# Performance work log

Measured on AMD Instinct MI355X. Metric: run time of the kernel, lower is better.

Reference implementation:

```python
import jax, jax.numpy as jnp
import numpy as np

B, S, T, H, E, V = 64, 128, 64, 512, 256, 10000


def setup_inputs() -> dict:
    key = jax.random.key(0)
    ks = jax.random.split(key, 16)
    w = 0.05
    return {
        "trg": jax.random.randint(ks[0], (B, T), 0, V),
        "encoder_hidden": jax.random.normal(ks[1], (B, S, 2 * H), jnp.float32),
        "src_lengths": jax.random.randint(ks[2], (B,), 1, S + 1),
        "h0": jax.random.normal(ks[3], (B, H), jnp.float32),
        "c0": jax.random.normal(ks[4], (B, H), jnp.float32),
        "emb_table": jax.random.normal(ks[5], (V, E), jnp.float32) * w,
        "Wkey": jax.random.normal(ks[6], (2 * H, H), jnp.float32) * w,      # attention.key_layer
        "Wquery": jax.random.normal(ks[7], (H, H), jnp.float32) * w,        # attention.query_layer
        "we": jax.random.normal(ks[8], (H,), jnp.float32) * w,              # attention.energy_layer
        "W_ih": jax.random.normal(ks[9], (4 * H, E + 2 * H), jnp.float32) * w,
        "W_hh": jax.random.normal(ks[10], (4 * H, H), jnp.float32) * w,
        "b_ih": jnp.zeros((4 * H,), jnp.float32),
        "b_hh": jnp.zeros((4 * H,), jnp.float32),
        "Wpre": jax.random.normal(ks[11], (3 * H + E, H), jnp.float32) * w,  # pre_output_layer (no bias)
        "Wgen": jax.random.normal(ks[12], (H, V), jnp.float32) * w,          # generator / softmax head
    }


def reference(trg, encoder_hidden, src_lengths, h0, c0, emb_table, Wkey, Wquery,
              we, W_ih, W_hh, b_ih, b_hh, Wpre, Wgen):
    # Teacher-forced unroll (teacher_forcing=True branch); dropout in eval mode.
    s = encoder_hidden.shape[1]
    proj_key = encoder_hidden @ Wkey                            # [B,S,H]
    mask = jnp.arange(s)[None, :] < src_lengths[:, None]        # [B,S]
    embs = emb_table[trg]                                       # [B,T,E]

    def step(carry, emb_t):
        h, c = carry                                            # [B,H] each
        q = h @ Wquery                                          # query = last-layer hidden
        e = jnp.einsum('bsh,h->bs', jnp.tanh(q[:, None, :] + proj_key), we)
        a = jax.nn.softmax(jnp.where(mask, e, -1e9), axis=-1)   # masked attention
        ctx = jnp.einsum('bs,bsd->bd', a, encoder_hidden)       # [B,2H]
        x = jnp.concatenate([emb_t, ctx], axis=-1)              # rnn_input
        g = x @ W_ih.T + h @ W_hh.T + b_ih + b_hh
        i_g, f_g, g_g, o_g = jnp.split(g, 4, axis=-1)           # torch LSTM gate order
        c_new = jax.nn.sigmoid(f_g) * c + jax.nn.sigmoid(i_g) * jnp.tanh(g_g)
        h_new = jax.nn.sigmoid(o_g) * jnp.tanh(c_new)
        pre = jnp.concatenate([emb_t, h_new, ctx], axis=-1) @ Wpre
        logp = jax.nn.log_softmax(pre @ Wgen, axis=-1)          # [B,V]
        return (h_new, c_new), logp

    (hf, cf), out = jax.lax.scan(step, (h0, c0), jnp.swapaxes(embs, 0, 1))
    return jnp.transpose(out, (1, 2, 0)), hf, cf                # out: [B,V,T]
```

## Files before the change

### kernel.cpp

```cpp
#include <hip/hip_runtime.h>

#define B 64
#define S 128
#define T 64
#define H 512
#define E 256
#define V 10000
#define H2 1024
#define G4 2048
#define KX 1536
#define KP 1792
#define VP 10112
#define NROW 4096

typedef unsigned short u16;
typedef __attribute__((ext_vector_type(8))) short bf16x8;
typedef __attribute__((ext_vector_type(4))) short bf16x4;
typedef __attribute__((ext_vector_type(4))) float floatx4;

__device__ inline float b2f(u16 h){
  union { unsigned int u; float f; } v; v.u = ((unsigned int)h) << 16; return v.f;
}
__device__ inline u16 f2b(float f){
  union { unsigned int u; float f; } v; v.f = f;
  unsigned int r = v.u + 0x7FFFu + ((v.u >> 16) & 1u);
  return (u16)(r >> 16);
}
__device__ __forceinline__ float rcpf(float x){ return __builtin_amdgcn_rcpf(x); }
__device__ inline float sigf(float x){ return rcpf(1.f + __expf(-x)); }
__device__ inline float tanh_fast(float x){ float e=__expf(2.f*x); return 1.f - 2.f*rcpf(e+1.f); }

__device__ __forceinline__ void st_wt_u32(u16* p, unsigned v){
  asm volatile("global_store_dword %0, %1, off sc0 sc1" :: "v"(p), "v"(v) : "memory");
}
__device__ __forceinline__ void st_wt_u16(u16* p, unsigned v){
  asm volatile("global_store_short %0, %1, off sc0 sc1" :: "v"(p), "v"(v) : "memory");
}
__device__ __forceinline__ unsigned ld_if(unsigned* p){
  unsigned v;
  asm volatile("global_load_dword %0, %1, off sc0 sc1\ns_waitcnt vmcnt(0)" : "=v"(v) : "v"(p) : "memory");
  return v;
}
__device__ __forceinline__ void st_if(unsigned* p, unsigned v){
  asm volatile("global_store_dword %0, %1, off sc0 sc1\ns_waitcnt vmcnt(0)" :: "v"(p), "v"(v) : "memory");
}

#define BAR_WORDS (128*64)

__global__ void k_cast(const float* __restrict__ src, u16* __restrict__ dst, int n){
  int i = blockIdx.x*256 + threadIdx.x;
  if (i < n) dst[i] = f2b(src[i]);
}
__global__ void k_tct(const float* __restrict__ src, u16* __restrict__ dst, int R, int C){
  __shared__ float tile[64][65];
  int c0 = blockIdx.x*64, r0 = blockIdx.y*64;
  int tid = threadIdx.x;
  #pragma unroll
  for (int i=0;i<16;i++){
    int flat = i*256 + tid;
    int rr = flat >> 6, cc = flat & 63;
    int c = c0 + cc;
    tile[rr][cc] = (c < C) ? src[(size_t)(r0+rr)*C + c] : 0.f;
  }
  __syncthreads();
  #pragma unroll
  for (int i=0;i<16;i++){
    int flat = i*256 + tid;
    int cc = flat >> 6, rr = flat & 63;
    dst[(size_t)(c0+cc)*R + r0 + rr] = f2b(tile[rr][cc]);
  }
}
__global__ void k_wch(const float* __restrict__ wih, const float* __restrict__ whh, u16* __restrict__ o){
  int i = blockIdx.x*256 + threadIdx.x;
  if (i < G4*KX){
    int gp = i / KX, k = i % KX;
    int j = gp >> 2, gate = gp & 3, g = gate*H + j;
    float v = (k < H2) ? wih[(size_t)g*(E+H2) + E + k] : whh[(size_t)g*H + (k - H2)];
    o[i] = f2b(v);
  }
}
__global__ void k_wihe(const float* __restrict__ wih, u16* __restrict__ o){
  int i = blockIdx.x*256 + threadIdx.x;
  if (i < G4*E){
    int gp = i / E, e = i % E;
    int j = gp >> 2, gate = gp & 3, g = gate*H + j;
    o[i] = f2b(wih[(size_t)g*(E+H2) + e]);
  }
}
__global__ void k_bias(const float* __restrict__ bi, const float* __restrict__ bh, float* __restrict__ o){
  int i = blockIdx.x*256 + threadIdx.x;
  if (i < G4){
    int j = i >> 2, gate = i & 3, g = gate*H + j;
    o[i] = bi[g] + bh[g];
  }
}
__global__ void k_emb(const int* __restrict__ trg, const float* __restrict__ emb, u16* __restrict__ catp){
  int i = blockIdx.x*256 + threadIdx.x;
  if (i < NROW*E){
    int row = i >> 8, e = i & 255;
    int tok = trg[row];
    catp[(size_t)row*KP + e] = f2b(emb[(size_t)tok*E + e]);
  }
}
__global__ void k_init(const float* __restrict__ h0, u16* __restrict__ xgs){
  int i = blockIdx.x*256 + threadIdx.x;
  if (i < B*H){
    int b = i >> 9, j = i & 511;
    xgs[(size_t)b*KX + H2 + j] = f2b(h0[i]);
  }
}
__global__ void k_zero(unsigned* bar){
  int i = blockIdx.x*256 + threadIdx.x;
  if (i < BAR_WORDS) bar[i] = 0u;
}
__global__ void k_lse(const float* __restrict__ sep, float* __restrict__ lse){
  int r = blockIdx.x*256 + threadIdx.x;
  if (r < NROW){
    float s = 0.f;
    for (int i=0;i<79;i++) s += sep[(size_t)r*80 + i];
    lse[r] = logf(s);
  }
}

template<int TN, int EPI>
__global__ __launch_bounds__(256) void gemm_bf16(
    const u16* __restrict__ A, int lda,
    const u16* __restrict__ BT, int ldb,
    int K,
    u16* outb, int ldc,
    float* sep,
    float* outp, const float* lse)
{
  constexpr int NSUB = TN/16;
  constexpr int NB = TN/64;
  __shared__ u16 sA[64*32];
  __shared__ u16 sB[TN*32];
  __shared__ float Cx[(EPI==3) ? 128*65 : 1];
  __shared__ float lseb[(EPI==3)?64:1];

  const int tid = threadIdx.x;
  const int lane = tid & 63;
  const int wv = tid >> 6;
  const int row0 = blockIdx.x * 64;
  const int n0 = blockIdx.y * TN;

  floatx4 acc[NSUB];
  #pragma unroll
  for (int s=0;s<NSUB;s++) acc[s] = (floatx4){0.f,0.f,0.f,0.f};

  const int ar = tid >> 2;
  const int ch = tid & 3;
  const int swz = (ar >> 1) & 3;
  const int px = ((lane & 15) >> 1) & 3;

  const u16* gA = A + (size_t)(row0+ar)*lda + ch*8;
  bf16x8 pa = *(const bf16x8*)gA;
  bf16x8 pb[NB];
  #pragma unroll
  for (int i=0;i<NB;i++) pb[i] = *(const bf16x8*)(BT + (size_t)(n0+i*64+ar)*ldb + ch*8);

  for (int k0 = 0; k0 < K; k0 += 32){
    __syncthreads();
    *(bf16x8*)&sA[ar*32 + ((ch ^ swz)*8)] = pa;
    #pragma unroll
    for (int i=0;i<NB;i++)
      *(bf16x8*)&sB[(i*64+ar)*32 + ((ch ^ swz)*8)] = pb[i];
    __syncthreads();
    if (k0 + 32 < K){
      pa = *(const bf16x8*)(gA + k0 + 32);
      #pragma unroll
      for (int i=0;i<NB;i++) pb[i] = *(const bf16x8*)(BT + (size_t)(n0+i*64+ar)*ldb + k0+32 + ch*8);
    }
    bf16x8 af = *(const bf16x8*)&sA[(16*wv + (lane&15))*32 + (((lane>>4) ^ px)*8)];
    #pragma unroll
    for (int s=0;s<NSUB;s++){
      bf16x8 bfv = *(const bf16x8*)&sB[(16*s + (lane&15))*32 + (((lane>>4) ^ px)*8)];
      acc[s] = __builtin_amdgcn_mfma_f32_16x16x32_bf16(af, bfv, acc[s], 0, 0, 0);
    }
  }

  if constexpr (EPI == 0 || EPI == 4){
    #pragma unroll
    for (int s=0;s<NSUB;s++)
      #pragma unroll
      for (int r=0;r<4;r++){
        int row = row0 + 16*wv + ((lane>>4)<<2) + r;
        int col = n0 + 16*s + (lane&15);
        if (EPI == 4) row = ((row & 63) << 6) | (row >> 6);
        outb[(size_t)row*ldc + col] = f2b(acc[s][r]);
      }
  }
  if constexpr (EPI == 2){
    float sr[4] = {0.f,0.f,0.f,0.f};
    #pragma unroll
    for (int s=0;s<NSUB;s++){
      int col = n0 + 16*s + (lane&15);
      if (col < V){
        #pragma unroll
        for (int r=0;r<4;r++) sr[r] += __expf(acc[s][r]);
      }
    }
    #pragma unroll
    for (int r=0;r<4;r++){
      float v = sr[r];
      v += __shfl_xor(v,1); v += __shfl_xor(v,2); v += __shfl_xor(v,4); v += __shfl_xor(v,8);
      sr[r] = v;
    }
    if ((lane&15)==0){
      #pragma unroll
      for (int r=0;r<4;r++){
        int row = row0 + 16*wv + ((lane>>4)<<2) + r;
        sep[(size_t)row*80 + blockIdx.y] = sr[r];
      }
    }
  }
  if constexpr (EPI == 3){
    #pragma unroll
    for (int s=0;s<NSUB;s++)
      #pragma unroll
      for (int r=0;r<4;r++){
        int rl = 16*wv + ((lane>>4)<<2) + r;
        int cl = 16*s + (lane&15);
        Cx[cl*65 + rl] = acc[s][r];
      }
    if (tid < 64) lseb[tid] = lse[row0 + tid];
    __syncthreads();
    int b = blockIdx.x;
    for (int idx = tid; idx < TN*16; idx += 256){
      int vl = idx >> 4, q4 = idx & 15;
      int v = n0 + vl;
      if (v < V){
        floatx4 o;
        o[0] = Cx[vl*65 + q4*4+0] - lseb[q4*4+0];
        o[1] = Cx[vl*65 + q4*4+1] - lseb[q4*4+1];
        o[2] = Cx[vl*65 + q4*4+2] - lseb[q4*4+2];
        o[3] = Cx[vl*65 + q4*4+3] - lseb[q4*4+3];
        *(floatx4*)&outp[((size_t)b*V + v)*T + q4*4] = o;
      }
    }
  }
}

__device__ __forceinline__ void wait_flags(unsigned* base, unsigned g){
  if (threadIdx.x < 64){
    unsigned* p = base + (unsigned)threadIdx.x*64;
    int it = 0;
    while (ld_if(p) < g && ++it < 5000000) asm volatile("s_sleep 1":::);
  }
  __syncthreads();
}

__global__ __launch_bounds__(512) void decoder_loop(
    u16* __restrict__ xgs, const float* __restrict__ c0f, float* __restrict__ outp,
    const u16* __restrict__ pk, const u16* __restrict__ encb,
    const float* __restrict__ we, const int* __restrict__ lens,
    const u16* __restrict__ wqT, u16* __restrict__ cph,
    const u16* __restrict__ wch, const u16* __restrict__ gembt,
    const float* __restrict__ bias, unsigned* __restrict__ bar)
{
  __shared__ u16 sA[64*128];
  __shared__ u16 sB[32*128];
  __shared__ float Cx[64*36];
  __shared__ u16 hsb[H];
  __shared__ __align__(16) float qw[H];
  __shared__ __align__(16) float wel[H];
  __shared__ float ep[512];
  __shared__ float ev[S], al[S];
  __shared__ float smax, sinv;

  const int tid = threadIdx.x, lane = tid & 63, wv = tid >> 6;
  const int blk = blockIdx.x;
  const int xcd = blk & 7, slot = blk >> 3;
  unsigned* flag_ctx = bar;
  unsigned* flag_h   = bar + 64*64;

  if (slot < 8){
    const int b = xcd*8 + slot;
    const int lenb = lens[b];
    wel[tid] = we[tid];
    __syncthreads();

    for (int t=0; t<T; t++){
      wait_flags(flag_h, (unsigned)t);
      u16* xgt = xgs + (size_t)t*B*KX;
      hsb[tid] = xgt[b*KX + H2 + tid];
      __syncthreads();
      {
        floatx4 accq[4];
        #pragma unroll
        for (int s=0;s<4;s++) accq[s] = (floatx4){0.f,0.f,0.f,0.f};
        const int kc = (lane>>4)*8;
        #pragma unroll 4
        for (int ks=0; ks<16; ks++){
          bf16x8 af = *(const bf16x8*)&hsb[ks*32 + kc];
          #pragma unroll
          for (int s=0;s<4;s++){
            const u16* bp = wqT + (size_t)(wv*64 + s*16 + (lane&15))*H + ks*32 + kc;
            accq[s] = __builtin_amdgcn_mfma_f32_16x16x32_bf16(af, *(const bf16x8*)bp, accq[s], 0, 0, 0);
          }
        }
        if (lane < 16){
          #pragma unroll
          for (int s=0;s<4;s++) qw[wv*64 + s*16 + lane] = accq[s][0];
        }
      }
      __syncthreads();
      {
        int s = tid >> 2, part = tid & 3;
        float a0 = 0.f;
        if (s < lenb){
          const u16* pr = pk + (size_t)(b*S + s)*H;
          #pragma unroll 4
          for (int m=0;m<16;m++){
            int k0 = part*8 + m*32;
            bf16x8 p8 = *(const bf16x8*)(pr + k0);
            floatx4 qa = *(const floatx4*)&qw[k0];
            floatx4 qb = *(const floatx4*)&qw[k0+4];
            floatx4 wa = *(const floatx4*)&wel[k0];
            floatx4 wb = *(const floatx4*)&wel[k0+4];
            #pragma unroll
            for (int i=0;i<4;i++){
              a0 += tanh_fast(qa[i] + b2f((u16)p8[i]))   * wa[i];
              a0 += tanh_fast(qb[i] + b2f((u16)p8[i+4])) * wb[i];
            }
          }
        }
        ep[tid] = a0;
      }
      __syncthreads();
      if (tid < S){
        float e = ep[tid*4] + ep[tid*4+1] + ep[tid*4+2] + ep[tid*4+3];
        ev[tid] = (tid < lenb) ? e : -1e30f;
      }
      __syncthreads();
      if (tid < 64){
        float m = fmaxf(ev[tid], ev[tid+64]);
        #pragma unroll
        for (int o=32;o>=1;o>>=1) m = fmaxf(m, __shfl_xor(m,o));
        if (tid==0) smax = m;
      }
      __syncthreads();
      if (tid < S) al[tid] = __expf(ev[tid]-smax);
      __syncthreads();
      if (tid < 64){
        float s2 = al[tid] + al[tid+64];
        #pragma unroll
        for (int o=32;o>=1;o>>=1) s2 += __shfl_xor(s2,o);
        if (tid==0) sinv = rcpf(s2);
      }
      __syncthreads();
      {
        float cx0=0.f, cx1=0.f;
        int d = tid*2;
        const u16* er = encb + (size_t)(b*S)*H2 + d;
        for (int ss=0; ss<lenb; ss++){
          unsigned int u = *(const unsigned int*)(er + (size_t)ss*H2);
          float a = al[ss];
          cx0 += a * b2f((u16)(u & 0xFFFFu));
          cx1 += a * b2f((u16)(u >> 16));
        }
        cx0 *= sinv; cx1 *= sinv;
        unsigned pack = ((unsigned)f2b(cx1) << 16) | (unsigned)f2b(cx0);
        st_wt_u32(xgt + (size_t)b*KX + d, pack);
        *(unsigned*)&cph[(size_t)(b*T + t)*KP + E + H + d] = pack;
      }
      asm volatile("s_waitcnt vmcnt(0)" ::: "memory");
      __syncthreads();
      if (tid == 0) st_if(flag_ctx + (unsigned)b*64, (unsigned)(t+1));
      __syncthreads();
    }
  } else {
    const int g = slot - 8;
    const int gid = xcd*8 + g;
    const int n0 = xcd*256 + g*32;
    const int kh = wv >> 2, wr = wv & 3;
    const int rs0 = tid >> 4, gs = tid & 15;
    const int rowa = 16*wr + (lane & 15);
    const int pb_ = tid >> 3, jl = tid & 7;
    const int jglob = (n0 >> 2) + jl;
    float creg = c0f[pb_*H + jglob];
    floatx4 bias4 = *(const floatx4*)(bias + n0 + jl*4);

    for (int t=0; t<T; t++){
      wait_flags(flag_ctx, (unsigned)(t+1));
      const u16* xgt = xgs + (size_t)t*B*KX;
      u16* xgn = xgs + (size_t)(t+1)*B*KX;
      bf16x4 g4 = *(const bf16x4*)(gembt + (size_t)(t*B + pb_)*G4 + n0 + jl*4);

      floatx4 acc[2];
      acc[0] = (floatx4){0.f,0.f,0.f,0.f};
      acc[1] = (floatx4){0.f,0.f,0.f,0.f};
      bf16x8 a0 = *(const bf16x8*)(xgt + (size_t)rs0*KX + gs*8);
      bf16x8 a1 = *(const bf16x8*)(xgt + (size_t)(rs0+32)*KX + gs*8);
      bf16x8 b0 = *(const bf16x8*)(wch + (size_t)(n0+rs0)*KX + gs*8);

      for (int kk=0; kk<12; kk++){
        __syncthreads();
        *(bf16x8*)&sA[rs0*128 + ((gs ^ (rs0&7))*8)] = a0;
        *(bf16x8*)&sA[(rs0+32)*128 + ((gs ^ (rs0&7))*8)] = a1;
        *(bf16x8*)&sB[rs0*128 + ((gs ^ (rs0&7))*8)] = b0;
        __syncthreads();
        if (kk < 11){
          int ko = (kk+1)*128;
          a0 = *(const bf16x8*)(xgt + (size_t)rs0*KX + ko + gs*8);
          a1 = *(const bf16x8*)(xgt + (size_t)(rs0+32)*KX + ko + gs*8);
          b0 = *(const bf16x8*)(wch + (size_t)(n0+rs0)*KX + ko + gs*8);
        }
        #pragma unroll
        for (int ks=0; ks<2; ks++){
          int gq = kh*8 + ks*4 + (lane>>4);
          bf16x8 af = *(const bf16x8*)&sA[rowa*128 + ((gq ^ (rowa&7))*8)];
          #pragma unroll
          for (int s=0;s<2;s++){
            int rowb = 16*s + (lane & 15);
            bf16x8 bfv = *(const bf16x8*)&sB[rowb*128 + ((gq ^ (rowb&7))*8)];
            acc[s] = __builtin_amdgcn_mfma_f32_16x16x32_bf16(af, bfv, acc[s], 0, 0, 0);
          }
        }
      }
      {
        int r0 = 16*wr + ((lane>>4)<<2);
        if (kh == 1){
          #pragma unroll
          for (int s=0;s<2;s++)
            #pragma unroll
            for (int r=0;r<4;r++) Cx[(r0+r)*36 + 16*s + (lane&15)] = acc[s][r];
        }
      }
      __syncthreads();
      {
        int r0 = 16*wr + ((lane>>4)<<2);
        if (kh == 0){
          #pragma unroll
          for (int s=0;s<2;s++)
            #pragma unroll
            for (int r=0;r<4;r++) Cx[(r0+r)*36 + 16*s + (lane&15)] += acc[s][r];
        }
      }
      __syncthreads();
      {
        float gi = Cx[pb_*36 + jl*4+0] + b2f((u16)g4[0]) + bias4[0];
        float gf = Cx[pb_*36 + jl*4+1] + b2f((u16)g4[1]) + bias4[1];
        float gg = Cx[pb_*36 + jl*4+2] + b2f((u16)g4[2]) + bias4[2];
        float go = Cx[pb_*36 + jl*4+3] + b2f((u16)g4[3]) + bias4[3];
        float cn = sigf(gf)*creg + sigf(gi)*tanhf(gg);
        float hn = sigf(go)*tanhf(cn);
        creg = cn;
        u16 hb = f2b(hn);
        st_wt_u16(xgn + (size_t)pb_*KX + H2 + jglob, (unsigned)hb);
        cph[(size_t)(pb_*T + t)*KP + E + jglob] = hb;
        if (t == T-1){
          outp[(size_t)B*V*T + pb_*H + jglob] = hn;
          outp[(size_t)B*V*T + B*H + pb_*H + jglob] = cn;
        }
      }
      asm volatile("s_waitcnt vmcnt(0)" ::: "memory");
      __syncthreads();
      if (tid == 0) st_if(flag_h + (unsigned)gid*64, (unsigned)(t+1));
      __syncthreads();
    }
  }
}

static inline int cdiv(int a, int b){ return (a + b - 1) / b; }

extern "C" void kernel_launch(void* const* d_in, const int* in_sizes, int n_in,
                              void* d_out, int out_size, void* d_ws, size_t ws_size,
                              hipStream_t stream)
{
  (void)in_sizes; (void)n_in; (void)out_size; (void)ws_size;
  const int*   trg  = (const int*)d_in[0];
  const float* enc  = (const float*)d_in[1];
  const int*   lens = (const int*)d_in[2];
  const float* h0   = (const float*)d_in[3];
  const float* c0   = (const float*)d_in[4];
  const float* embt = (const float*)d_in[5];
  const float* wkey = (const float*)d_in[6];
  const float* wqry = (const float*)d_in[7];
  const float* we   = (const float*)d_in[8];
  const float* wih  = (const float*)d_in[9];
  const float* whh  = (const float*)d_in[10];
  const float* bi   = (const float*)d_in[11];
  const float* bh   = (const float*)d_in[12];
  const float* wpre = (const float*)d_in[13];
  const float* wgen = (const float*)d_in[14];
  float* out = (float*)d_out;

  char* p = (char*)d_ws;
  auto carve = [&](size_t bytes)->char*{ char* r = p; p += (bytes + 255) & ~(size_t)255; return r; };
  u16*   encb  = (u16*)  carve((size_t)B*S*H2*2);
  u16*   pkb   = (u16*)  carve((size_t)B*S*H*2);
  u16*   catp  = (u16*)  carve((size_t)NROW*KP*2);
  u16*   gembb = (u16*)  carve((size_t)NROW*G4*2);
  u16*   preb  = (u16*)  carve((size_t)NROW*H*2);
  u16*   wgt   = (u16*)  carve((size_t)VP*H*2);
  u16*   wch   = (u16*)  carve((size_t)G4*KX*2);
  u16*   wihe  = (u16*)  carve((size_t)G4*E*2);
  u16*   wkeyT = (u16*)  carve((size_t)H*H2*2);
  u16*   wqT   = (u16*)  carve((size_t)H*H*2);
  u16*   wpreT = (u16*)  carve((size_t)H*KP*2);
  u16*   xgs   = (u16*)  carve((size_t)(T+1)*B*KX*2);
  float* biasp = (float*)carve((size_t)G4*4);
  float* sep   = (float*)carve((size_t)NROW*80*4);
  float* lse   = (float*)carve((size_t)NROW*4);
  unsigned* bar = (unsigned*)carve(BAR_WORDS*4);

  k_cast<<<cdiv(B*S*H2,256),256,0,stream>>>(enc, encb, B*S*H2);
  k_tct<<<dim3(H/64, H/64),256,0,stream>>>(wqry, wqT, H, H);
  k_tct<<<dim3(H/64, H2/64),256,0,stream>>>(wkey, wkeyT, H2, H);
  k_tct<<<dim3(H/64, KP/64),256,0,stream>>>(wpre, wpreT, KP, H);
  k_tct<<<dim3(VP/64, H/64),256,0,stream>>>(wgen, wgt, H, V);
  k_wch<<<cdiv(G4*KX,256),256,0,stream>>>(wih, whh, wch);
  k_wihe<<<cdiv(G4*E,256),256,0,stream>>>(wih, wihe);
  k_bias<<<cdiv(G4,256),256,0,stream>>>(bi, bh, biasp);
  k_emb<<<cdiv(NROW*E,256),256,0,stream>>>(trg, embt, catp);
  k_init<<<cdiv(B*H,256),256,0,stream>>>(h0, xgs);
  k_zero<<<cdiv(BAR_WORDS,256),256,0,stream>>>(bar);

  gemm_bf16<64,0><<<dim3(B*S/64, H/64),256,0,stream>>>(
      encb, H2, wkeyT, H2, H2, pkb, H, nullptr, nullptr, nullptr);
  gemm_bf16<64,4><<<dim3(NROW/64, G4/64),256,0,stream>>>(
      catp, KP, wihe, E, E, gembb, G4, nullptr, nullptr, nullptr);

  decoder_loop<<<128,512,0,stream>>>(xgs, c0, out, pkb, encb, we, lens,
                                     wqT, catp, wch, gembb, biasp, bar);

  gemm_bf16<64,0><<<dim3(NROW/64, H/64),256,0,stream>>>(
      catp, KP, wpreT, KP, KP, preb, H, nullptr, nullptr, nullptr);

  gemm_bf16<128,2><<<dim3(NROW/64, VP/128),256,0,stream>>>(
      preb, H, wgt, H, H, nullptr, 0, sep, nullptr, nullptr);
  k_lse<<<cdiv(NROW,256),256,0,stream>>>(sep, lse);
  gemm_bf16<128,3><<<dim3(NROW/64, VP/128),256,0,stream>>>(
      preb, H, wgt, H, H, nullptr, 0, nullptr, out, lse);
}
```

Before: 2.501 ms.

## Merge attention and LSTM roles into one block per batch row with MFMA context

The persistent decoder kernel used to split 128 blocks into attention blocks and LSTM-gate blocks that handed data back and forth through flags. It now runs 64 blocks, each doing attention for one batch row and then a 32-column slice of the gate GEMM. The recurrent h-part of the gate GEMM is computed before waiting for all context flags, so it overlaps with other blocks finishing attention. The context reduction now runs as bf16 MFMA against a pre-transposed encoder copy instead of a scalar loop. The trade-offs are an extra transpose kernel and workspace buffer, half as many CUs in use, attention weights rounded to bf16, and fast tanh in the gate update.

```diff
diff --git a/kernel.cpp b/kernel.cpp
--- a/kernel.cpp
+++ b/kernel.cpp
@@ -68,6 +68,24 @@
     int flat = i*256 + tid;
     int cc = flat >> 6, rr = flat & 63;
     dst[(size_t)(c0+cc)*R + r0 + rr] = f2b(tile[rr][cc]);
+  }
+}
+__global__ void k_encT(const float* __restrict__ enc, u16* __restrict__ o){
+  __shared__ float tile[64][65];
+  int d0 = blockIdx.x*64, s0 = blockIdx.y*64, b = blockIdx.z;
+  int tid = threadIdx.x;
+  #pragma unroll
+  for (int i=0;i<16;i++){
+    int flat = i*256 + tid;
+    int sl = flat >> 6, dl = flat & 63;
+    tile[sl][dl] = enc[((size_t)(b*S) + s0+sl)*H2 + d0+dl];
+  }
+  __syncthreads();
+  #pragma unroll
+  for (int i=0;i<16;i++){
+    int flat = i*256 + tid;
+    int dl = flat >> 6, sl = flat & 63;
+    o[((size_t)b*H2 + d0+dl)*S + s0+sl] = f2b(tile[sl][dl]);
   }
 }
 __global__ void k_wch(const float* __restrict__ wih, const float* __restrict__ whh, u16* __restrict__ o){
@@ -252,7 +270,7 @@
 
 __global__ __launch_bounds__(512) void decoder_loop(
     u16* __restrict__ xgs, const float* __restrict__ c0f, float* __restrict__ outp,
-    const u16* __restrict__ pk, const u16* __restrict__ encb,
+    const u16* __restrict__ pk, const u16* __restrict__ encbT,
     const float* __restrict__ we, const int* __restrict__ lens,
     const u16* __restrict__ wqT, u16* __restrict__ cph,
     const u16* __restrict__ wch, const u16* __restrict__ gembt,
@@ -261,140 +279,148 @@
   __shared__ u16 sA[64*128];
   __shared__ u16 sB[32*128];
   __shared__ float Cx[64*36];
-  __shared__ u16 hsb[H];
+  __shared__ __align__(16) u16 hsb[H];
   __shared__ __align__(16) float qw[H];
   __shared__ __align__(16) float wel[H];
   __shared__ float ep[512];
-  __shared__ float ev[S], al[S];
+  __shared__ float ev[S];
+  __shared__ __align__(16) u16 alb[S];
+  __shared__ __align__(16) float ctxf[H2];
   __shared__ float smax, sinv;
 
   const int tid = threadIdx.x, lane = tid & 63, wv = tid >> 6;
   const int blk = blockIdx.x;
-  const int xcd = blk & 7, slot = blk >> 3;
+  const int b = blk;
+  const int lenb = lens[b];
   unsigned* flag_ctx = bar;
   unsigned* flag_h   = bar + 64*64;
 
-  if (slot < 8){
-    const int b = xcd*8 + slot;
-    const int lenb = lens[b];
-    wel[tid] = we[tid];
-    __syncthreads();
-
-    for (int t=0; t<T; t++){
-      wait_flags(flag_h, (unsigned)t);
-      u16* xgt = xgs + (size_t)t*B*KX;
-      hsb[tid] = xgt[b*KX + H2 + tid];
-      __syncthreads();
-      {
-        floatx4 accq[4];
-        #pragma unroll
-        for (int s=0;s<4;s++) accq[s] = (floatx4){0.f,0.f,0.f,0.f};
-        const int kc = (lane>>4)*8;
+  const int n0 = blk*32;
+  const int kh = wv >> 2, wr = wv & 3;
+  const int rs0 = tid >> 4, gs = tid & 15;
+  const int rowa = 16*wr + (lane & 15);
+  const int pb_ = tid >> 3, jl = tid & 7;
+  const int jglob = n0/4 + jl;
+  float creg = c0f[pb_*H + jglob];
+  floatx4 bias4 = *(const floatx4*)(bias + n0 + jl*4);
+
+  wel[tid] = we[tid];
+  __syncthreads();
+
+  for (int t=0; t<T; t++){
+    u16* xgt = xgs + (size_t)t*B*KX;
+    u16* xgn = xgs + (size_t)(t+1)*B*KX;
+
+    wait_flags(flag_h, (unsigned)t);
+    hsb[tid] = xgt[b*KX + H2 + tid];
+    __syncthreads();
+
+    {
+      floatx4 accq[4];
+      #pragma unroll
+      for (int s=0;s<4;s++) accq[s] = (floatx4){0.f,0.f,0.f,0.f};
+      const int kc = (lane>>4)*8;
+      #pragma unroll 4
+      for (int ks=0; ks<16; ks++){
+        bf16x8 af = *(const bf16x8*)&hsb[ks*32 + kc];
+        #pragma unroll
+        for (int s=0;s<4;s++){
+          const u16* bp = wqT + (size_t)(wv*64 + s*16 + (lane&15))*H + ks*32 + kc;
+          accq[s] = __builtin_amdgcn_mfma_f32_16x16x32_bf16(af, *(const bf16x8*)bp, accq[s], 0, 0, 0);
+        }
+      }
+      if (lane < 16){
+        #pragma unroll
+        for (int s=0;s<4;s++) qw[wv*64 + s*16 + lane] = accq[s][0];
+      }
+    }
+    __syncthreads();
+
+    {
+      int s = tid >> 2, part = tid & 3;
+      float a0 = 0.f;
+      if (s < lenb){
+        const u16* pr = pk + (size_t)(b*S + s)*H;
         #pragma unroll 4
-        for (int ks=0; ks<16; ks++){
-          bf16x8 af = *(const bf16x8*)&hsb[ks*32 + kc];
+        for (int m=0;m<16;m++){
+          int k0 = part*8 + m*32;
+          bf16x8 p8 = *(const bf16x8*)(pr + k0);
+          floatx4 qa = *(const floatx4*)&qw[k0];
+          floatx4 qb = *(const floatx4*)&qw[k0+4];
+          floatx4 wa = *(const floatx4*)&wel[k0];
+          floatx4 wb = *(const floatx4*)&wel[k0+4];
           #pragma unroll
-          for (int s=0;s<4;s++){
-            const u16* bp = wqT + (size_t)(wv*64 + s*16 + (lane&15))*H + ks*32 + kc;
-            accq[s] = __builtin_amdgcn_mfma_f32_16x16x32_bf16(af, *(const bf16x8*)bp, accq[s], 0, 0, 0);
+          for (int i=0;i<4;i++){
+            a0 += tanh_fast(qa[i] + b2f((u16)p8[i]))   * wa[i];
+            a0 += tanh_fast(qb[i] + b2f((u16)p8[i+4])) * wb[i];
           }
         }
-        if (lane < 16){
-          #pragma unroll
-          for (int s=0;s<4;s++) qw[wv*64 + s*16 + lane] = accq[s][0];
-        }
-      }
-      __syncthreads();
-      {
-        int s = tid >> 2, part = tid & 3;
-        float a0 = 0.f;
-        if (s < lenb){
-          const u16* pr = pk + (size_t)(b*S + s)*H;
-          #pragma unroll 4
-          for (int m=0;m<16;m++){
-            int k0 = part*8 + m*32;
-            bf16x8 p8 = *(const bf16x8*)(pr + k0);
-            floatx4 qa = *(const floatx4*)&qw[k0];
-            floatx4 qb = *(const floatx4*)&qw[k0+4];
-            floatx4 wa = *(const floatx4*)&wel[k0];
-            floatx4 wb = *(const floatx4*)&wel[k0+4];
-            #pragma unroll
-            for (int i=0;i<4;i++){
-              a0 += tanh_fast(qa[i] + b2f((u16)p8[i]))   * wa[i];
-              a0 += tanh_fast(qb[i] + b2f((u16)p8[i+4])) * wb[i];
-            }
-          }
-        }
-        ep[tid] = a0;
-      }
-      __syncthreads();
-      if (tid < S){
-        float e = ep[tid*4] + ep[tid*4+1] + ep[tid*4+2] + ep[tid*4+3];
-        ev[tid] = (tid < lenb) ? e : -1e30f;
-      }
-      __syncthreads();
-      if (tid < 64){
-        float m = fmaxf(ev[tid], ev[tid+64]);
-        #pragma unroll
-        for (int o=32;o>=1;o>>=1) m = fmaxf(m, __shfl_xor(m,o));
-        if (tid==0) smax = m;
-      }
-      __syncthreads();
-      if (tid < S) al[tid] = __expf(ev[tid]-smax);
-      __syncthreads();
-      if (tid < 64){
-        float s2 = al[tid] + al[tid+64];
-        #pragma unroll
-        for (int o=32;o>=1;o>>=1) s2 += __shfl_xor(s2,o);
-        if (tid==0) sinv = rcpf(s2);
-      }
-      __syncthreads();
-      {
-        float cx0=0.f, cx1=0.f;
-        int d = tid*2;
-        const u16* er = encb + (size_t)(b*S)*H2 + d;
-        for (int ss=0; ss<lenb; ss++){
-          unsigned int u = *(const unsigned int*)(er + (size_t)ss*H2);
-          float a = al[ss];
-          cx0 += a * b2f((u16)(u & 0xFFFFu));
-          cx1 += a * b2f((u16)(u >> 16));
-        }
-        cx0 *= sinv; cx1 *= sinv;
-        unsigned pack = ((unsigned)f2b(cx1) << 16) | (unsigned)f2b(cx0);
-        st_wt_u32(xgt + (size_t)b*KX + d, pack);
-        *(unsigned*)&cph[(size_t)(b*T + t)*KP + E + H + d] = pack;
-      }
-      asm volatile("s_waitcnt vmcnt(0)" ::: "memory");
-      __syncthreads();
-      if (tid == 0) st_if(flag_ctx + (unsigned)b*64, (unsigned)(t+1));
-      __syncthreads();
-    }
-  } else {
-    const int g = slot - 8;
-    const int gid = xcd*8 + g;
-    const int n0 = xcd*256 + g*32;
-    const int kh = wv >> 2, wr = wv & 3;
-    const int rs0 = tid >> 4, gs = tid & 15;
-    const int rowa = 16*wr + (lane & 15);
-    const int pb_ = tid >> 3, jl = tid & 7;
-    const int jglob = (n0 >> 2) + jl;
-    float creg = c0f[pb_*H + jglob];
-    floatx4 bias4 = *(const floatx4*)(bias + n0 + jl*4);
-
-    for (int t=0; t<T; t++){
-      wait_flags(flag_ctx, (unsigned)(t+1));
-      const u16* xgt = xgs + (size_t)t*B*KX;
-      u16* xgn = xgs + (size_t)(t+1)*B*KX;
-      bf16x4 g4 = *(const bf16x4*)(gembt + (size_t)(t*B + pb_)*G4 + n0 + jl*4);
-
-      floatx4 acc[2];
-      acc[0] = (floatx4){0.f,0.f,0.f,0.f};
-      acc[1] = (floatx4){0.f,0.f,0.f,0.f};
-      bf16x8 a0 = *(const bf16x8*)(xgt + (size_t)rs0*KX + gs*8);
-      bf16x8 a1 = *(const bf16x8*)(xgt + (size_t)(rs0+32)*KX + gs*8);
-      bf16x8 b0 = *(const bf16x8*)(wch + (size_t)(n0+rs0)*KX + gs*8);
-
-      for (int kk=0; kk<12; kk++){
+      }
+      ep[tid] = a0;
+    }
+    __syncthreads();
+    if (tid < S){
+      float e = ep[tid*4] + ep[tid*4+1] + ep[tid*4+2] + ep[tid*4+3];
+      ev[tid] = (tid < lenb) ? e : -1e30f;
+    }
+    __syncthreads();
+    if (tid < 64){
+      float m = fmaxf(ev[tid], ev[tid+64]);
+      #pragma unroll
+      for (int o=32;o>=1;o>>=1) m = fmaxf(m, __shfl_xor(m,o));
+      if (tid==0) smax = m;
+    }
+    __syncthreads();
+    if (tid < S) ev[tid] = __expf(ev[tid]-smax);
+    __syncthreads();
+    if (tid < 64){
+      float s2 = ev[tid] + ev[tid+64];
+      #pragma unroll
+      for (int o=32;o>=1;o>>=1) s2 += __shfl_xor(s2,o);
+      if (tid==0) sinv = rcpf(s2);
+    }
+    __syncthreads();
+    if (tid < S) alb[tid] = f2b(ev[tid]*sinv);
+    __syncthreads();
+
+    {
+      floatx4 accc[8];
+      #pragma unroll
+      for (int s=0;s<8;s++) accc[s] = (floatx4){0.f,0.f,0.f,0.f};
+      const int kc = (lane>>4)*8;
+      #pragma unroll
+      for (int ks=0; ks<4; ks++){
+        bf16x8 af = *(const bf16x8*)&alb[ks*32 + kc];
+        #pragma unroll
+        for (int s8=0;s8<8;s8++){
+          const u16* bp = encbT + ((size_t)b*H2 + wv*128 + s8*16 + (lane&15))*S + ks*32 + kc;
+          accc[s8] = __builtin_amdgcn_mfma_f32_16x16x32_bf16(af, *(const bf16x8*)bp, accc[s8], 0, 0, 0);
+        }
+      }
+      if (lane < 16){
+        #pragma unroll
+        for (int s8=0;s8<8;s8++) ctxf[wv*128 + s8*16 + lane] = accc[s8][0];
+      }
+    }
+    __syncthreads();
+    {
+      int d = tid*2;
+      unsigned pack = ((unsigned)f2b(ctxf[d+1]) << 16) | (unsigned)f2b(ctxf[d]);
+      st_wt_u32(xgt + (size_t)b*KX + d, pack);
+      *(unsigned*)&cph[(size_t)(b*T + t)*KP + E + H + d] = pack;
+    }
+    asm volatile("s_waitcnt vmcnt(0)" ::: "memory");
+    __syncthreads();
+    if (tid == 0) st_if(flag_ctx + (unsigned)b*64, (unsigned)(t+1));
+
+    floatx4 gacc[2];
+    gacc[0] = (floatx4){0.f,0.f,0.f,0.f};
+    gacc[1] = (floatx4){0.f,0.f,0.f,0.f};
+    {
+      bf16x8 a0 = *(const bf16x8*)(xgt + (size_t)rs0*KX + 1024 + gs*8);
+      bf16x8 a1 = *(const bf16x8*)(xgt + (size_t)(rs0+32)*KX + 1024 + gs*8);
+      bf16x8 b0 = *(const bf16x8*)(wch + (size_t)(n0+rs0)*KX + 1024 + gs*8);
+      for (int kk=8; kk<12; kk++){
         __syncthreads();
         *(bf16x8*)&sA[rs0*128 + ((gs ^ (rs0&7))*8)] = a0;
         *(bf16x8*)&sA[(rs0+32)*128 + ((gs ^ (rs0&7))*8)] = a1;
@@ -414,51 +440,83 @@
           for (int s=0;s<2;s++){
             int rowb = 16*s + (lane & 15);
             bf16x8 bfv = *(const bf16x8*)&sB[rowb*128 + ((gq ^ (rowb&7))*8)];
-            acc[s] = __builtin_amdgcn_mfma_f32_16x16x32_bf16(af, bfv, acc[s], 0, 0, 0);
+            gacc[s] = __builtin_amdgcn_mfma_f32_16x16x32_bf16(af, bfv, gacc[s], 0, 0, 0);
           }
         }
       }
-      {
-        int r0 = 16*wr + ((lane>>4)<<2);
-        if (kh == 1){
+    }
+
+    wait_flags(flag_ctx, (unsigned)(t+1));
+    {
+      bf16x8 a0 = *(const bf16x8*)(xgt + (size_t)rs0*KX + gs*8);
+      bf16x8 a1 = *(const bf16x8*)(xgt + (size_t)(rs0+32)*KX + gs*8);
+      bf16x8 b0 = *(const bf16x8*)(wch + (size_t)(n0+rs0)*KX + gs*8);
+      for (int kk=0; kk<8; kk++){
+        __syncthreads();
+        *(bf16x8*)&sA[rs0*128 + ((gs ^ (rs0&7))*8)] = a0;
+        *(bf16x8*)&sA[(rs0+32)*128 + ((gs ^ (rs0&7))*8)] = a1;
+        *(bf16x8*)&sB[rs0*128 + ((gs ^ (rs0&7))*8)] = b0;
+        __syncthreads();
+        if (kk < 7){
+          int ko = (kk+1)*128;
+          a0 = *(const bf16x8*)(xgt + (size_t)rs0*KX + ko + gs*8);
+          a1 = *(const bf16x8*)(xgt + (size_t)(rs0+32)*KX + ko + gs*8);
+          b0 = *(const bf16x8*)(wch + (size_t)(n0+rs0)*KX + ko + gs*8);
+        }
+        #pragma unroll
+        for (int ks=0; ks<2; ks++){
+          int gq = kh*8 + ks*4 + (lane>>4);
+          bf16x8 af = *(const bf16x8*)&sA[rowa*128 + ((gq ^ (rowa&7))*8)];
           #pragma unroll
-          for (int s=0;s<2;s++)
-            #pragma unroll
-            for (int r=0;r<4;r++) Cx[(r0+r)*36 + 16*s + (lane&15)] = acc[s][r];
-        }
-      }
-      __syncthreads();
-      {
-        int r0 = 16*wr + ((lane>>4)<<2);
-        if (kh == 0){
+          for (int s=0;s<2;s++){
+            int rowb = 16*s + (lane & 15);
+            bf16x8 bfv = *(const bf16x8*)&sB[rowb*128 + ((gq ^ (rowb&7))*8)];
+            gacc[s] = __builtin_amdgcn_mfma_f32_16x16x32_bf16(af, bfv, gacc[s], 0, 0, 0);
+          }
+        }
+      }
+    }
+    {
+      int r0 = 16*wr + ((lane>>4)<<2);
+      if (kh == 1){
+        #pragma unroll
+        for (int s=0;s<2;s++)
           #pragma unroll
-          for (int s=0;s<2;s++)
-            #pragma unroll
-            for (int r=0;r<4;r++) Cx[(r0+r)*36 + 16*s + (lane&15)] += acc[s][r];
-        }
-      }
-      __syncthreads();
-      {
-        float gi = Cx[pb_*36 + jl*4+0] + b2f((u16)g4[0]) + bias4[0];
-        float gf = Cx[pb_*36 + jl*4+1] + b2f((u16)g4[1]) + bias4[1];
-        float gg = Cx[pb_*36 + jl*4+2] + b2f((u16)g4[2]) + bias4[2];
-        float go = Cx[pb_*36 + jl*4+3] + b2f((u16)g4[3]) + bias4[3];
-        float cn = sigf(gf)*creg + sigf(gi)*tanhf(gg);
-        float hn = sigf(go)*tanhf(cn);
-        creg = cn;
-        u16 hb = f2b(hn);
-        st_wt_u16(xgn + (size_t)pb_*KX + H2 + jglob, (unsigned)hb);
-        cph[(size_t)(pb_*T + t)*KP + E + jglob] = hb;
-        if (t == T-1){
-          outp[(size_t)B*V*T + pb_*H + jglob] = hn;
-          outp[(size_t)B*V*T + B*H + pb_*H + jglob] = cn;
-        }
-      }
-      asm volatile("s_waitcnt vmcnt(0)" ::: "memory");
-      __syncthreads();
-      if (tid == 0) st_if(flag_h + (unsigned)gid*64, (unsigned)(t+1));
-      __syncthreads();
-    }
+          for (int r=0;r<4;r++) Cx[(r0+r)*36 + 16*s + (lane&15)] = gacc[s][r];
+      }
+    }
+    __syncthreads();
+    {
+      int r0 = 16*wr + ((lane>>4)<<2);
+      if (kh == 0){
+        #pragma unroll
+        for (int s=0;s<2;s++)
+          #pragma unroll
+          for (int r=0;r<4;r++) Cx[(r0+r)*36 + 16*s + (lane&15)] += gacc[s][r];
+      }
+    }
+    __syncthreads();
+    {
+      bf16x4 g4 = *(const bf16x4*)(gembt + (size_t)(t*B + pb_)*G4 + n0 + jl*4);
+      float gi = Cx[pb_*36 + jl*4+0] + b2f((u16)g4[0]) + bias4[0];
+      float gf = Cx[pb_*36 + jl*4+1] + b2f((u16)g4[1]) + bias4[1];
+      float gg = Cx[pb_*36 + jl*4+2] + b2f((u16)g4[2]) + bias4[2];
+      float go = Cx[pb_*36 + jl*4+3] + b2f((u16)g4[3]) + bias4[3];
+      float cn = sigf(gf)*creg + sigf(gi)*tanh_fast(gg);
+      float hn = sigf(go)*tanh_fast(cn);
+      creg = cn;
+      u16 hb = f2b(hn);
+      st_wt_u16(xgn + (size_t)pb_*KX + H2 + jglob, (unsigned)hb);
+      cph[(size_t)(pb_*T + t)*KP + E + jglob] = hb;
+      if (t == T-1){
+        outp[(size_t)B*V*T + pb_*H + jglob] = hn;
+        outp[(size_t)B*V*T + B*H + pb_*H + jglob] = cn;
+      }
+    }
+    asm volatile("s_waitcnt vmcnt(0)" ::: "memory");
+    __syncthreads();
+    if (tid == 0) st_if(flag_h + (unsigned)blk*64, (unsigned)(t+1));
+    __syncthreads();
   }
 }
 
@@ -489,6 +547,7 @@
   char* p = (char*)d_ws;
   auto carve = [&](size_t bytes)->char*{ char* r = p; p += (bytes + 255) & ~(size_t)255; return r; };
   u16*   encb  = (u16*)  carve((size_t)B*S*H2*2);
+  u16*   encbT = (u16*)  carve((size_t)B*H2*S*2);
   u16*   pkb   = (u16*)  carve((size_t)B*S*H*2);
   u16*   catp  = (u16*)  carve((size_t)NROW*KP*2);
   u16*   gembb = (u16*)  carve((size_t)NROW*G4*2);
@@ -506,6 +565,7 @@
   unsigned* bar = (unsigned*)carve(BAR_WORDS*4);
 
   k_cast<<<cdiv(B*S*H2,256),256,0,stream>>>(enc, encb, B*S*H2);
+  k_encT<<<dim3(H2/64, S/64, B),256,0,stream>>>(enc, encbT);
   k_tct<<<dim3(H/64, H/64),256,0,stream>>>(wqry, wqT, H, H);
   k_tct<<<dim3(H/64, H2/64),256,0,stream>>>(wkey, wkeyT, H2, H);
   k_tct<<<dim3(H/64, KP/64),256,0,stream>>>(wpre, wpreT, KP, H);
@@ -522,8 +582,8 @@
   gemm_bf16<64,4><<<dim3(NROW/64, G4/64),256,0,stream>>>(
       catp, KP, wihe, E, E, gembb, G4, nullptr, nullptr, nullptr);
 
-  decoder_loop<<<128,512,0,stream>>>(xgs, c0, out, pkb, encb, we, lens,
-                                     wqT, catp, wch, gembb, biasp, bar);
+  decoder_loop<<<64,512,0,stream>>>(xgs, c0, out, pkb, encbT, we, lens,
+                                    wqT, catp, wch, gembb, biasp, bar);
 
   gemm_bf16<64,0><<<dim3(NROW/64, H/64),256,0,stream>>>(
       catp, KP, wpreT, KP, KP, preb, H, nullptr, nullptr, nullptr);
```

After: 3.092 ms. +23.6%, slower.
